# Kernel optimization log

Measured on AMD Instinct MI355X. Metric: run time of the kernel, lower is better.

Reference implementation:

```python
import jax, jax.numpy as jnp
import numpy as np

LATENT, U_DIM, NUM_PROD, NUM_INJ, FEAT_C = 128, 30, 20, 10, 128
WELL_IN = LATENT + U_DIM + FEAT_C  # 286
HID = 64
B = 16384


def setup_inputs() -> dict:
    key = jax.random.key(0)
    ks = jax.random.split(key, 12)
    s = lambda fan_in: 1.0 / np.sqrt(fan_in)
    return {
        "zt": jax.random.normal(ks[0], (B, LATENT), jnp.float32),
        "dt": 1,
        "ut": jax.random.normal(ks[1], (B, U_DIM), jnp.float32),
        "well_features": jax.random.normal(ks[2], (B, NUM_PROD, FEAT_C), jnp.float32),
        # StructuredODEFunc params: dz/dt = -(L L^T) z + Bm u
        "L": jax.random.normal(ks[3], (LATENT, LATENT), jnp.float32) * s(LATENT),
        "Bm": jax.random.normal(ks[4], (LATENT, U_DIM), jnp.float32) * s(U_DIM),
        # per-well MLP heads, stacked: [P, in, out]
        "W1": jax.random.uniform(ks[5], (NUM_PROD, WELL_IN, HID), jnp.float32, -s(WELL_IN), s(WELL_IN)),
        "b1": jax.random.uniform(ks[6], (NUM_PROD, HID), jnp.float32, -s(WELL_IN), s(WELL_IN)),
        "W2": jax.random.uniform(ks[7], (NUM_PROD, HID, 2), jnp.float32, -s(HID), s(HID)),
        "b2": jax.random.uniform(ks[8], (NUM_PROD, 2), jnp.float32, -s(HID), s(HID)),
        # injector head: Linear(latent+u_dim, num_inj)
        "Wi": jax.random.uniform(ks[9], (LATENT + U_DIM, NUM_INJ), jnp.float32, -s(LATENT + U_DIM), s(LATENT + U_DIM)),
        "bi": jax.random.uniform(ks[10], (NUM_INJ,), jnp.float32, -s(LATENT + U_DIM), s(LATENT + U_DIM)),
    }


def reference(zt, dt, ut, well_features, L, Bm, W1, b1, W2, b2, Wi, bi):
    # ODE step: A = -L L^T, f(z) = A z + Bm u; euler over t_span [0,1] -> one step h=1
    A = -(L @ L.T)                                  # [D, D]
    zt1 = zt + zt @ A.T + ut @ Bm.T                 # [B, D]
    zu = jnp.concatenate([zt1, ut], axis=-1)        # [B, D+U]
    # per-well heads, fused as batched gather-MLP
    zu_b = jnp.broadcast_to(zu[:, None, :], (zu.shape[0], NUM_PROD, zu.shape[1]))
    head_in = jnp.concatenate([zu_b, well_features], axis=-1)        # [B, P, WELL_IN]
    h = jax.nn.relu(jnp.einsum('bpi,pih->bph', head_in, W1) + b1)    # [B, P, 64]
    well_out = jnp.einsum('bph,pho->bpo', h, W2) + b2                # [B, P, 2]
    well_out = well_out.reshape(well_out.shape[0], NUM_PROD * 2)     # concat order matches loop
    inj_out = zu @ Wi + bi                                           # [B, num_inj]
    yt1 = jnp.concatenate([well_out, inj_out], axis=-1)              # [B, 2P+I]
    return zt1, yt1
```

## Files before the change

kernel.cpp:

```cpp
#include <hip/hip_runtime.h>

#define BATCH   16384
#define LATENT  128
#define U_DIM   30
#define NUM_PROD 20
#define NUM_INJ 10
#define FEAT_C  128
#define WELL_IN 286
#define HID     64
#define ZT1_N   (BATCH*LATENT)
#define OUT_ROW (NUM_PROD*2+NUM_INJ)

typedef unsigned short u16;
typedef __attribute__((ext_vector_type(8))) short  short8;
typedef __attribute__((ext_vector_type(4))) float  floatx4;

__device__ __forceinline__ u16 f2bf(float f){
    unsigned x = __builtin_bit_cast(unsigned, f);
    x += 0x7fffu + ((x >> 16) & 1u);
    return (u16)(x >> 16);
}
__device__ __forceinline__ short8 cvt8(floatx4 a, floatx4 b){
    short8 s;
    s[0]=(short)f2bf(a[0]); s[1]=(short)f2bf(a[1]);
    s[2]=(short)f2bf(a[2]); s[3]=(short)f2bf(a[3]);
    s[4]=(short)f2bf(b[0]); s[5]=(short)f2bf(b[1]);
    s[6]=(short)f2bf(b[2]); s[7]=(short)f2bf(b[3]);
    return s;
}

#define NW1  368640
#define NGS  20480
#define NWIS 2560
#define NW2S 20480
__device__ u16 g_w1s[NW1];
__device__ u16 g_gs [NGS];
__device__ u16 g_wis[NWIS];
__device__ u16 g_w2s[NW2S];
__device__ u16 g_zub[BATCH * 160];

__global__ __launch_bounds__(256) void prep_kernel(
    const float* __restrict__ L, const float* __restrict__ Bm,
    const float* __restrict__ W1, const float* __restrict__ Wi,
    const float* __restrict__ W2)
{
    const int bx = blockIdx.x, t = threadIdx.x;
    if (bx < 1440) {
        int idx = bx*256 + t;
        int j = idx & 7, lane = (idx >> 3) & 63;
        int rest = idx >> 9;
        int kk = rest % 9, pn = rest / 9;
        int n0 = pn & 3, p = pn >> 2;
        int k = kk*32 + ((lane>>4)*8) + j;
        int n = n0*16 + (lane & 15);
        u16 v = 0;
        if (k < 158)        v = f2bf(W1[(p*WELL_IN + k)*HID + n]);
        else if (k >= 160)  v = f2bf(W1[(p*WELL_IN + (k-2))*HID + n]);
        g_w1s[idx] = v;
        return;
    }
    if (bx < 1532) {
        int sid = (bx-1440)*256 + t;
        if (sid < NW2S) {
            int j=sid&7, lane=(sid>>3)&63, rest=sid>>9;
            int kk=rest&1, p=rest>>1;
            int k=kk*32+((lane>>4)*8)+j, n=lane&15;
            g_w2s[sid] = (n<2) ? f2bf(W2[(p*HID+k)*2+n]) : (u16)0;
            return;
        }
        sid -= NW2S;
        if (sid < NWIS) {
            int j=sid&7, lane=(sid>>3)&63, kk=sid>>9;
            int k=kk*32+((lane>>4)*8)+j, n=lane&15;
            g_wis[sid] = (k<158 && n<NUM_INJ) ? f2bf(Wi[k*NUM_INJ+n]) : (u16)0;
            return;
        }
        sid -= NWIS;
        if (sid < 512) {
            int lane=sid&63, nt=sid>>6;
            int q=lane>>4, n=nt*16+(lane&15);
#pragma unroll
            for (int j = 0; j < 8; j++) {
                int u = q*8 + j;
                float v = (u < U_DIM) ? Bm[n*U_DIM + u] : 0.f;
                g_gs[((nt*5+4)*64 + lane)*8 + j] = f2bf(v);
            }
        }
        return;
    }
    const int mt = bx - 1532;
    const int w = t>>6, lane=t&63, q=lane>>4, m=lane&15;
    floatx4 accG[2];
    accG[0]=(floatx4){0.f,0.f,0.f,0.f}; accG[1]=(floatx4){0.f,0.f,0.f,0.f};
#pragma unroll
    for (int kk = 0; kk < 4; kk++) {
        const float* ap = &L[(mt*16+m)*128 + kk*32 + q*8];
        short8 a = cvt8(*(const floatx4*)ap, *(const floatx4*)(ap+4));
#pragma unroll
        for (int ntl = 0; ntl < 2; ntl++) {
            int nt = w*2 + ntl;
            const float* bp = &L[(nt*16+m)*128 + kk*32 + q*8];
            short8 b = cvt8(*(const floatx4*)bp, *(const floatx4*)(bp+4));
            accG[ntl] = __builtin_amdgcn_mfma_f32_16x16x32_bf16(a, b, accG[ntl], 0, 0, 0);
        }
    }
#pragma unroll
    for (int ntl = 0; ntl < 2; ntl++)
#pragma unroll
        for (int r = 0; r < 4; r++) {
            int kg = mt*16 + q*4 + r;
            int n  = (w*2+ntl)*16 + m;
            float v = ((kg==n) ? 1.f : 0.f) - accG[ntl][r];
            int fi = ((n>>4)*5 + (kg>>5))*512 + (((kg>>3)&3)*16 + (n&15))*8 + (kg&7);
            g_gs[fi] = f2bf(v);
        }
}

__global__ __launch_bounds__(256) void ker_zt1(
    const float* __restrict__ zt, const float* __restrict__ ut,
    float* __restrict__ outf)
{
    __shared__ alignas(16) u16 Xs[32][168];
    const int t = threadIdx.x;
    const int row0 = blockIdx.x * 32;

    for (int i = t; i < 1024; i += 256) {
        int r = i >> 5, c4 = i & 31;
        floatx4 v = *(const floatx4*)&zt[(row0 + r)*128 + c4*4];
        u16* d = &Xs[r][c4*4];
        d[0]=f2bf(v[0]); d[1]=f2bf(v[1]); d[2]=f2bf(v[2]); d[3]=f2bf(v[3]);
    }
    for (int i = t; i < 32*U_DIM; i += 256) {
        int r = i / U_DIM, c = i - r*U_DIM;
        u16 b = f2bf(ut[(row0 + r)*U_DIM + c]);
        Xs[r][128 + c] = b;
        g_zub[(row0 + r)*160 + 128 + c] = b;
    }
    if (t < 64) {
        int r = t >> 1, k = 158 + (t & 1);
        Xs[r][k] = 0;
        g_zub[(row0 + r)*160 + k] = 0;
    }
    __syncthreads();

    const int w = t >> 6, lane = t & 63, q = lane >> 4, m = lane & 15;
    const int mt = w & 1, ng = (w >> 1) * 4;

    floatx4 acc[4];
#pragma unroll
    for (int c = 0; c < 4; c++) acc[c] = (floatx4){0.f,0.f,0.f,0.f};
#pragma unroll
    for (int kk = 0; kk < 5; kk++) {
        short8 a = *(const short8*)&Xs[mt*16 + m][kk*32 + q*8];
#pragma unroll
        for (int c = 0; c < 4; c++) {
            short8 b = *(const short8*)&g_gs[(((ng+c)*5 + kk)*64 + lane)*8];
            acc[c] = __builtin_amdgcn_mfma_f32_16x16x32_bf16(a, b, acc[c], 0, 0, 0);
        }
    }
#pragma unroll
    for (int c = 0; c < 4; c++)
#pragma unroll
        for (int r = 0; r < 4; r++) {
            int row = row0 + mt*16 + q*4 + r;
            int col = (ng+c)*16 + m;
            float v = acc[c][r];
            outf[row*128 + col] = v;
            g_zub[row*160 + col] = f2bf(v);
        }
}

__global__ __launch_bounds__(256) void ker_wells(
    const float* __restrict__ wff, const float* __restrict__ b1,
    const float* __restrict__ b2,  const float* __restrict__ bi,
    float* __restrict__ outf)
{
    __shared__ alignas(16) u16 zus[32][168];
    __shared__ alignas(16) u16 hs[4][32][72];
    const int t = threadIdx.x;
    const int row0 = blockIdx.x * 32;
    const int w = t >> 6, lane = t & 63, q = lane >> 4, m = lane & 15;
    const int p = blockIdx.y * 4 + w;

    floatx4 wfv[2][4][2];
#pragma unroll
    for (int rt = 0; rt < 2; rt++)
#pragma unroll
        for (int kk = 0; kk < 4; kk++) {
            const float* pb = &wff[((row0 + rt*16 + m)*NUM_PROD + p)*FEAT_C + kk*32 + q*8];
            wfv[rt][kk][0] = *(const floatx4*)pb;
            wfv[rt][kk][1] = *(const floatx4*)(pb + 4);
        }

    for (int i = t; i < 640; i += 256) {
        int r = i / 20, c8 = i - r*20;
        *(short8*)&zus[r][c8*8] = *(const short8*)&g_zub[(row0 + r)*160 + c8*8];
    }
    __syncthreads();

    short8 za[2][5];
#pragma unroll
    for (int rt = 0; rt < 2; rt++)
#pragma unroll
        for (int kk = 0; kk < 5; kk++)
            za[rt][kk] = *(const short8*)&zus[rt*16 + m][kk*32 + q*8];

    short8 wa[2][4];
#pragma unroll
    for (int rt = 0; rt < 2; rt++)
#pragma unroll
        for (int kk = 0; kk < 4; kk++)
            wa[rt][kk] = cvt8(wfv[rt][kk][0], wfv[rt][kk][1]);

    floatx4 acc[2][4];
#pragma unroll
    for (int rt = 0; rt < 2; rt++)
#pragma unroll
        for (int n0 = 0; n0 < 4; n0++) acc[rt][n0] = (floatx4){0.f,0.f,0.f,0.f};
    const u16* w1p = g_w1s + (size_t)p * 4 * 9 * 64 * 8;
#pragma unroll
    for (int kk = 0; kk < 9; kk++) {
        short8 a0 = (kk < 5) ? za[0][kk] : wa[0][kk-5];
        short8 a1 = (kk < 5) ? za[1][kk] : wa[1][kk-5];
#pragma unroll
        for (int n0 = 0; n0 < 4; n0++) {
            short8 b = *(const short8*)&w1p[((n0*9 + kk)*64 + lane)*8];
            acc[0][n0] = __builtin_amdgcn_mfma_f32_16x16x32_bf16(a0, b, acc[0][n0], 0, 0, 0);
            acc[1][n0] = __builtin_amdgcn_mfma_f32_16x16x32_bf16(a1, b, acc[1][n0], 0, 0, 0);
        }
    }

    if (blockIdx.y == 0 && w < 2) {
        floatx4 ai = (floatx4){0.f,0.f,0.f,0.f};
#pragma unroll
        for (int kk = 0; kk < 5; kk++) {
            short8 b = *(const short8*)&g_wis[(kk*64 + lane)*8];
            ai = __builtin_amdgcn_mfma_f32_16x16x32_bf16(za[w][kk], b, ai, 0, 0, 0);
        }
        if (m < NUM_INJ) {
            float bv = bi[m];
#pragma unroll
            for (int r = 0; r < 4; r++) {
                int row = row0 + 16*w + q*4 + r;
                outf[ZT1_N + row*OUT_ROW + 40 + m] = ai[r] + bv;
            }
        }
    }

#pragma unroll
    for (int n0 = 0; n0 < 4; n0++) {
        float bb = b1[p*HID + n0*16 + m];
#pragma unroll
        for (int rt = 0; rt < 2; rt++)
#pragma unroll
            for (int r = 0; r < 4; r++) {
                float v = acc[rt][n0][r] + bb;
                v = v > 0.f ? v : 0.f;
                hs[w][rt*16 + q*4 + r][n0*16 + m] = f2bf(v);
            }
    }

    floatx4 a2[2];
    a2[0] = (floatx4){0.f,0.f,0.f,0.f};
    a2[1] = (floatx4){0.f,0.f,0.f,0.f};
#pragma unroll
    for (int rt = 0; rt < 2; rt++)
#pragma unroll
        for (int kk2 = 0; kk2 < 2; kk2++) {
            short8 a = *(const short8*)&hs[w][rt*16 + m][kk2*32 + q*8];
            short8 b = *(const short8*)&g_w2s[((p*2 + kk2)*64 + lane)*8];
            a2[rt] = __builtin_amdgcn_mfma_f32_16x16x32_bf16(a, b, a2[rt], 0, 0, 0);
        }
    if (m < 2) {
        float bb = b2[p*2 + m];
#pragma unroll
        for (int rt = 0; rt < 2; rt++)
#pragma unroll
            for (int r = 0; r < 4; r++) {
                int row = row0 + rt*16 + q*4 + r;
                outf[ZT1_N + row*OUT_ROW + p*2 + m] = a2[rt][r] + bb;
            }
    }
}

extern "C" void kernel_launch(void* const* d_in, const int* in_sizes, int n_in,
                              void* d_out, int out_size, void* d_ws, size_t ws_size,
                              hipStream_t stream)
{
    const float* zt = (const float*)d_in[0];
    const float* ut = (const float*)d_in[2];
    const float* wf = (const float*)d_in[3];
    const float* L  = (const float*)d_in[4];
    const float* Bm = (const float*)d_in[5];
    const float* W1 = (const float*)d_in[6];
    const float* b1 = (const float*)d_in[7];
    const float* W2 = (const float*)d_in[8];
    const float* b2 = (const float*)d_in[9];
    const float* Wi = (const float*)d_in[10];
    const float* bi = (const float*)d_in[11];
    float* outf = (float*)d_out;

    prep_kernel<<<1540, 256, 0, stream>>>(L, Bm, W1, Wi, W2);
    ker_zt1<<<BATCH/32, 256, 0, stream>>>(zt, ut, outf);
    ker_wells<<<dim3(512, 5), 256, 0, stream>>>(wf, b1, b2, bi, outf);
}
```

Baseline: 337.3 us.

## Fuse zt1 and well-head kernels into one with double-buffered feature loads

Merges the ODE-step kernel and the per-well MLP kernel into a single kernel. Each block now computes zt1 in shared memory and loops over five wells per wave, so the bf16 zu round-trip through global memory and one launch go away. Well features for the next well are prefetched into registers while the current one computes. Outputs are staged in shared memory and written as coalesced vector stores. The grid shrinks from 2560 to 512 blocks and each wave holds more registers, which lowers parallelism and occupancy.

```diff
diff --git a/kernel.cpp b/kernel.cpp
--- a/kernel.cpp
+++ b/kernel.cpp
@@ -37,7 +37,6 @@
 __device__ u16 g_gs [NGS];
 __device__ u16 g_wis[NWIS];
 __device__ u16 g_w2s[NW2S];
-__device__ u16 g_zub[BATCH * 160];
 
 __global__ __launch_bounds__(256) void prep_kernel(
     const float* __restrict__ L, const float* __restrict__ Bm,
@@ -116,170 +115,172 @@
         }
 }
 
-__global__ __launch_bounds__(256) void ker_zt1(
+__global__ __launch_bounds__(256) void ker_main(
     const float* __restrict__ zt, const float* __restrict__ ut,
-    float* __restrict__ outf)
-{
-    __shared__ alignas(16) u16 Xs[32][168];
-    const int t = threadIdx.x;
-    const int row0 = blockIdx.x * 32;
-
-    for (int i = t; i < 1024; i += 256) {
-        int r = i >> 5, c4 = i & 31;
-        floatx4 v = *(const floatx4*)&zt[(row0 + r)*128 + c4*4];
-        u16* d = &Xs[r][c4*4];
-        d[0]=f2bf(v[0]); d[1]=f2bf(v[1]); d[2]=f2bf(v[2]); d[3]=f2bf(v[3]);
-    }
-    for (int i = t; i < 32*U_DIM; i += 256) {
-        int r = i / U_DIM, c = i - r*U_DIM;
-        u16 b = f2bf(ut[(row0 + r)*U_DIM + c]);
-        Xs[r][128 + c] = b;
-        g_zub[(row0 + r)*160 + 128 + c] = b;
-    }
-    if (t < 64) {
-        int r = t >> 1, k = 158 + (t & 1);
-        Xs[r][k] = 0;
-        g_zub[(row0 + r)*160 + k] = 0;
-    }
-    __syncthreads();
-
-    const int w = t >> 6, lane = t & 63, q = lane >> 4, m = lane & 15;
-    const int mt = w & 1, ng = (w >> 1) * 4;
-
-    floatx4 acc[4];
-#pragma unroll
-    for (int c = 0; c < 4; c++) acc[c] = (floatx4){0.f,0.f,0.f,0.f};
-#pragma unroll
-    for (int kk = 0; kk < 5; kk++) {
-        short8 a = *(const short8*)&Xs[mt*16 + m][kk*32 + q*8];
-#pragma unroll
-        for (int c = 0; c < 4; c++) {
-            short8 b = *(const short8*)&g_gs[(((ng+c)*5 + kk)*64 + lane)*8];
-            acc[c] = __builtin_amdgcn_mfma_f32_16x16x32_bf16(a, b, acc[c], 0, 0, 0);
-        }
-    }
-#pragma unroll
-    for (int c = 0; c < 4; c++)
-#pragma unroll
-        for (int r = 0; r < 4; r++) {
-            int row = row0 + mt*16 + q*4 + r;
-            int col = (ng+c)*16 + m;
-            float v = acc[c][r];
-            outf[row*128 + col] = v;
-            g_zub[row*160 + col] = f2bf(v);
-        }
-}
-
-__global__ __launch_bounds__(256) void ker_wells(
     const float* __restrict__ wff, const float* __restrict__ b1,
     const float* __restrict__ b2,  const float* __restrict__ bi,
     float* __restrict__ outf)
 {
-    __shared__ alignas(16) u16 zus[32][168];
-    __shared__ alignas(16) u16 hs[4][32][72];
+    __shared__ alignas(16) u16   zus[32][168];
+    __shared__ alignas(16) u16   hs[4][32][72];
+    __shared__ alignas(16) float outs[32][50];
     const int t = threadIdx.x;
     const int row0 = blockIdx.x * 32;
     const int w = t >> 6, lane = t & 63, q = lane >> 4, m = lane & 15;
-    const int p = blockIdx.y * 4 + w;
-
-    floatx4 wfv[2][4][2];
-#pragma unroll
-    for (int rt = 0; rt < 2; rt++)
-#pragma unroll
-        for (int kk = 0; kk < 4; kk++) {
-            const float* pb = &wff[((row0 + rt*16 + m)*NUM_PROD + p)*FEAT_C + kk*32 + q*8];
-            wfv[rt][kk][0] = *(const floatx4*)pb;
-            wfv[rt][kk][1] = *(const floatx4*)(pb + 4);
-        }
-
-    for (int i = t; i < 640; i += 256) {
-        int r = i / 20, c8 = i - r*20;
-        *(short8*)&zus[r][c8*8] = *(const short8*)&g_zub[(row0 + r)*160 + c8*8];
+
+    floatx4 wfvA[2][4][2], wfvB[2][4][2];
+    auto load_wf = [&](floatx4 (&buf)[2][4][2], int pp){
+        const int p = w*5 + pp;
+#pragma unroll
+        for (int rt = 0; rt < 2; rt++)
+#pragma unroll
+            for (int kk = 0; kk < 4; kk++) {
+                const float* pb = &wff[((size_t)(row0 + rt*16 + m)*NUM_PROD + p)*FEAT_C + kk*32 + q*8];
+                buf[rt][kk][0] = *(const floatx4*)pb;
+                buf[rt][kk][1] = *(const floatx4*)(pb + 4);
+            }
+    };
+    load_wf(wfvA, 0);
+
+    for (int i = t; i < 1024; i += 256) {
+        int r = i >> 5, c4 = i & 31;
+        floatx4 v = *(const floatx4*)&zt[(size_t)(row0 + r)*128 + c4*4];
+        u16* d = &zus[r][c4*4];
+        d[0]=f2bf(v[0]); d[1]=f2bf(v[1]); d[2]=f2bf(v[2]); d[3]=f2bf(v[3]);
+    }
+    for (int i = t; i < 32*U_DIM; i += 256) {
+        int r = i / U_DIM, c = i - r*U_DIM;
+        zus[r][128 + c] = f2bf(ut[(row0 + r)*U_DIM + c]);
+    }
+    if (t < 64) {
+        zus[t >> 1][158 + (t & 1)] = 0;
     }
     __syncthreads();
 
-    short8 za[2][5];
-#pragma unroll
-    for (int rt = 0; rt < 2; rt++)
-#pragma unroll
-        for (int kk = 0; kk < 5; kk++)
-            za[rt][kk] = *(const short8*)&zus[rt*16 + m][kk*32 + q*8];
-
-    short8 wa[2][4];
-#pragma unroll
-    for (int rt = 0; rt < 2; rt++)
-#pragma unroll
-        for (int kk = 0; kk < 4; kk++)
-            wa[rt][kk] = cvt8(wfv[rt][kk][0], wfv[rt][kk][1]);
-
-    floatx4 acc[2][4];
-#pragma unroll
-    for (int rt = 0; rt < 2; rt++)
-#pragma unroll
-        for (int n0 = 0; n0 < 4; n0++) acc[rt][n0] = (floatx4){0.f,0.f,0.f,0.f};
-    const u16* w1p = g_w1s + (size_t)p * 4 * 9 * 64 * 8;
-#pragma unroll
-    for (int kk = 0; kk < 9; kk++) {
-        short8 a0 = (kk < 5) ? za[0][kk] : wa[0][kk-5];
-        short8 a1 = (kk < 5) ? za[1][kk] : wa[1][kk-5];
-#pragma unroll
-        for (int n0 = 0; n0 < 4; n0++) {
-            short8 b = *(const short8*)&w1p[((n0*9 + kk)*64 + lane)*8];
-            acc[0][n0] = __builtin_amdgcn_mfma_f32_16x16x32_bf16(a0, b, acc[0][n0], 0, 0, 0);
-            acc[1][n0] = __builtin_amdgcn_mfma_f32_16x16x32_bf16(a1, b, acc[1][n0], 0, 0, 0);
-        }
-    }
-
-    if (blockIdx.y == 0 && w < 2) {
-        floatx4 ai = (floatx4){0.f,0.f,0.f,0.f};
+    {
+        const int mt = w & 1, ng = (w >> 1) * 4;
+        floatx4 acc[4];
+#pragma unroll
+        for (int c = 0; c < 4; c++) acc[c] = (floatx4){0.f,0.f,0.f,0.f};
+#pragma unroll
+        for (int kk = 0; kk < 5; kk++) {
+            short8 a = *(const short8*)&zus[mt*16 + m][kk*32 + q*8];
+#pragma unroll
+            for (int c = 0; c < 4; c++) {
+                short8 b = *(const short8*)&g_gs[(((ng+c)*5 + kk)*64 + lane)*8];
+                acc[c] = __builtin_amdgcn_mfma_f32_16x16x32_bf16(a, b, acc[c], 0, 0, 0);
+            }
+        }
+        __syncthreads();
+#pragma unroll
+        for (int c = 0; c < 4; c++)
+#pragma unroll
+            for (int r = 0; r < 4; r++) {
+                int row = mt*16 + q*4 + r;
+                int col = (ng+c)*16 + m;
+                float v = acc[c][r];
+                outf[(size_t)(row0 + row)*128 + col] = v;
+                zus[row][col] = f2bf(v);
+            }
+    }
+    __syncthreads();
+
+    if (w == 3) {
+        floatx4 ai[2];
+        ai[0]=(floatx4){0.f,0.f,0.f,0.f}; ai[1]=(floatx4){0.f,0.f,0.f,0.f};
 #pragma unroll
         for (int kk = 0; kk < 5; kk++) {
             short8 b = *(const short8*)&g_wis[(kk*64 + lane)*8];
-            ai = __builtin_amdgcn_mfma_f32_16x16x32_bf16(za[w][kk], b, ai, 0, 0, 0);
+#pragma unroll
+            for (int rt = 0; rt < 2; rt++) {
+                short8 a = *(const short8*)&zus[rt*16 + m][kk*32 + q*8];
+                ai[rt] = __builtin_amdgcn_mfma_f32_16x16x32_bf16(a, b, ai[rt], 0, 0, 0);
+            }
         }
         if (m < NUM_INJ) {
             float bv = bi[m];
 #pragma unroll
-            for (int r = 0; r < 4; r++) {
-                int row = row0 + 16*w + q*4 + r;
-                outf[ZT1_N + row*OUT_ROW + 40 + m] = ai[r] + bv;
-            }
-        }
-    }
-
-#pragma unroll
-    for (int n0 = 0; n0 < 4; n0++) {
-        float bb = b1[p*HID + n0*16 + m];
+            for (int rt = 0; rt < 2; rt++)
+#pragma unroll
+                for (int r = 0; r < 4; r++)
+                    outs[rt*16 + q*4 + r][40 + m] = ai[rt][r] + bv;
+        }
+    }
+
+    auto compute_well = [&](const floatx4 (&buf)[2][4][2], int pp){
+        const int p = w*5 + pp;
+        floatx4 acc[2][4];
 #pragma unroll
         for (int rt = 0; rt < 2; rt++)
 #pragma unroll
-            for (int r = 0; r < 4; r++) {
-                float v = acc[rt][n0][r] + bb;
-                v = v > 0.f ? v : 0.f;
-                hs[w][rt*16 + q*4 + r][n0*16 + m] = f2bf(v);
-            }
-    }
-
-    floatx4 a2[2];
-    a2[0] = (floatx4){0.f,0.f,0.f,0.f};
-    a2[1] = (floatx4){0.f,0.f,0.f,0.f};
-#pragma unroll
-    for (int rt = 0; rt < 2; rt++)
-#pragma unroll
-        for (int kk2 = 0; kk2 < 2; kk2++) {
-            short8 a = *(const short8*)&hs[w][rt*16 + m][kk2*32 + q*8];
-            short8 b = *(const short8*)&g_w2s[((p*2 + kk2)*64 + lane)*8];
-            a2[rt] = __builtin_amdgcn_mfma_f32_16x16x32_bf16(a, b, a2[rt], 0, 0, 0);
-        }
-    if (m < 2) {
-        float bb = b2[p*2 + m];
+            for (int n0 = 0; n0 < 4; n0++) acc[rt][n0] = (floatx4){0.f,0.f,0.f,0.f};
+        const u16* w1p = g_w1s + (size_t)p * 4 * 9 * 64 * 8;
+#pragma unroll
+        for (int kk = 0; kk < 9; kk++) {
+            short8 a0, a1;
+            if (kk < 5) {
+                a0 = *(const short8*)&zus[m][kk*32 + q*8];
+                a1 = *(const short8*)&zus[16 + m][kk*32 + q*8];
+            } else {
+                a0 = cvt8(buf[0][kk-5][0], buf[0][kk-5][1]);
+                a1 = cvt8(buf[1][kk-5][0], buf[1][kk-5][1]);
+            }
+#pragma unroll
+            for (int n0 = 0; n0 < 4; n0++) {
+                short8 b = *(const short8*)&w1p[((n0*9 + kk)*64 + lane)*8];
+                acc[0][n0] = __builtin_amdgcn_mfma_f32_16x16x32_bf16(a0, b, acc[0][n0], 0, 0, 0);
+                acc[1][n0] = __builtin_amdgcn_mfma_f32_16x16x32_bf16(a1, b, acc[1][n0], 0, 0, 0);
+            }
+        }
+#pragma unroll
+        for (int n0 = 0; n0 < 4; n0++) {
+            float bb = b1[p*HID + n0*16 + m];
+#pragma unroll
+            for (int rt = 0; rt < 2; rt++)
+#pragma unroll
+                for (int r = 0; r < 4; r++) {
+                    float v = acc[rt][n0][r] + bb;
+                    v = v > 0.f ? v : 0.f;
+                    hs[w][rt*16 + q*4 + r][n0*16 + m] = f2bf(v);
+                }
+        }
+        floatx4 a2[2];
+        a2[0]=(floatx4){0.f,0.f,0.f,0.f}; a2[1]=(floatx4){0.f,0.f,0.f,0.f};
 #pragma unroll
         for (int rt = 0; rt < 2; rt++)
 #pragma unroll
-            for (int r = 0; r < 4; r++) {
-                int row = row0 + rt*16 + q*4 + r;
-                outf[ZT1_N + row*OUT_ROW + p*2 + m] = a2[rt][r] + bb;
-            }
+            for (int kk2 = 0; kk2 < 2; kk2++) {
+                short8 a = *(const short8*)&hs[w][rt*16 + m][kk2*32 + q*8];
+                short8 b = *(const short8*)&g_w2s[((p*2 + kk2)*64 + lane)*8];
+                a2[rt] = __builtin_amdgcn_mfma_f32_16x16x32_bf16(a, b, a2[rt], 0, 0, 0);
+            }
+        if (m < 2) {
+            float bb = b2[p*2 + m];
+#pragma unroll
+            for (int rt = 0; rt < 2; rt++)
+#pragma unroll
+                for (int r = 0; r < 4; r++)
+                    outs[rt*16 + q*4 + r][p*2 + m] = a2[rt][r] + bb;
+        }
+    };
+
+#pragma unroll
+    for (int pp = 0; pp < 5; pp++) {
+        if ((pp & 1) == 0) {
+            if (pp < 4) load_wf(wfvB, pp+1);
+            compute_well(wfvA, pp);
+        } else {
+            if (pp < 4) load_wf(wfvA, pp+1);
+            compute_well(wfvB, pp);
+        }
+    }
+    __syncthreads();
+
+    {
+        const float* of = &outs[0][0];
+        float* dst = outf + (size_t)ZT1_N + (size_t)row0 * OUT_ROW;
+        for (int i = t; i < 400; i += 256)
+            *(floatx4*)&dst[i*4] = *(const floatx4*)&of[i*4];
     }
 }
 
@@ -301,6 +302,5 @@
     float* outf = (float*)d_out;
 
     prep_kernel<<<1540, 256, 0, stream>>>(L, Bm, W1, Wi, W2);
-    ker_zt1<<<BATCH/32, 256, 0, stream>>>(zt, ut, outf);
-    ker_wells<<<dim3(512, 5), 256, 0, stream>>>(wf, b1, b2, bi, outf);
-}
+    ker_main<<<512, 256, 0, stream>>>(zt, ut, wf, b1, b2, bi, outf);
+}
```

After: 288.9 us. -14.3%, faster.
